# Kernel optimization log

Measured on AMD Instinct MI355X. Metric: run time of the kernel, lower is better.

Reference implementation:

```python
import jax, jax.numpy as jnp
import numpy as np

NN_SIZE = 10  # __init__ default nn_size


def setup_inputs() -> dict:
    key = jax.random.key(0)
    k1, k2 = jax.random.split(key)
    B, N, C = 8, 4096, 3
    xyz1 = jax.random.normal(k1, (B, N, C), dtype=jnp.float32)
    # xyz2 is a small deformation of xyz1 (realistic: deformed shape, same topology)
    xyz2 = xyz1 + 0.05 * jax.random.normal(k2, (B, N, C), dtype=jnp.float32)
    return {"xyz1": xyz1, "xyz2": xyz2}


def _knn_idx(pts, k):
    # brute-force squared-euclidean KNN of pts to itself; pts: (B,N,3) -> idx (B,N,k)
    sq = jnp.sum(pts * pts, axis=-1)                             # (B,N)
    d = sq[:, :, None] - 2.0 * jnp.einsum('bnc,bmc->bnm', pts, pts) + sq[:, None, :]
    _, idx = jax.lax.top_k(-d, k)                                # smallest distances
    return idx


def _point_to_plane(xyz, idx, k):
    # gather neighbors, center, PCA normal from 10x3 SVD, signed point-to-plane dist
    B, N, C = xyz.shape
    grouped = jax.vmap(lambda p, i: p[i])(xyz, idx)              # (B,N,k,3)
    center = jnp.mean(grouped, axis=2, keepdims=True)            # (B,N,1,3)
    local = (grouped - center).reshape(B * N, k, C)              # (B*N,k,3)
    _, _, vh = jnp.linalg.svd(local, full_matrices=False)        # vh: (B*N,3,3)
    # torch V[:, :, -1] == row -1 of Vh: singular vector of smallest singular value
    normals = jax.lax.stop_gradient(vh[:, -1, :].reshape(B, N, C))
    return jnp.sum((xyz - center[:, :, 0, :]) * normals, axis=-1)  # (B,N)


def reference(xyz1, xyz2):
    idx = _knn_idx(xyz1, NN_SIZE)
    ptof1 = _point_to_plane(xyz1, idx, NN_SIZE)
    ptof2 = _point_to_plane(xyz2, idx, NN_SIZE)
    mse = lambda a, b: jnp.mean((a - b) ** 2)
    loss = mse(jnp.abs(ptof1), jnp.abs(ptof2))
    bent = jnp.maximum(ptof2 - ptof1, 0.0)
    loss = loss + 5.0 * mse(bent, jnp.zeros_like(bent))
    return loss
```

## Files before the change

kernel.cpp:

```cpp
#include <hip/hip_runtime.h>
#include <math.h>

#define BB   8
#define NN   4096
#define KK   10
#define TPB  256
#define NPTS (BB * NN)

#define GPP  16
#define PPB  (TPB / GPP)
#define BPBK (NN / PPB)
#define KNBLK (BB * BPBK)
#define TILE 512
#define CAP  32

#define SVDBLK 256
#define SBLK   256

#define LARTG_OLD 0
#define EPSV  5.9604644775390625e-8
#define UNFLV 1.1754943508222875e-38
#define TOLV (10.0 * EPSV)

static __device__ __forceinline__ double lapy2d(double x, double y) {
  double xa = fabs(x), ya = fabs(y);
  double w = fmax(xa, ya), z = fmin(xa, ya);
  if (z == 0.0) return w;
  double q = z / w;
  return w * sqrt(1.0 + q * q);
}

static __device__ __forceinline__ void lartg(double f, double g,
                                             double &c, double &s, double &r) {
#if LARTG_OLD
  if (g == 0.0) { c = 1.0; s = 0.0; r = f; }
  else if (f == 0.0) { c = 0.0; s = 1.0; r = g; }
  else {
    double d = sqrt(f * f + g * g);
    c = f / d; s = g / d; r = d;
    if (fabs(f) > fabs(g) && c < 0.0) { c = -c; s = -s; r = -r; }
  }
#else
  if (g == 0.0) { c = 1.0; s = 0.0; r = f; }
  else if (f == 0.0) { c = 0.0; s = copysign(1.0, g); r = fabs(g); }
  else {
    double d = sqrt(f * f + g * g);
    c = fabs(f) / d;
    r = copysign(d, f);
    s = g / r;
  }
#endif
}

static __device__ void las2(double f, double g, double h, double &ssmin, double &ssmax) {
  double fa = fabs(f), ga = fabs(g), ha = fabs(h);
  double fhmn = fmin(fa, ha), fhmx = fmax(fa, ha);
  if (fhmn == 0.0) {
    ssmin = 0.0;
    if (fhmx == 0.0) ssmax = ga;
    else {
      double mn = fmin(fhmx, ga), mx = fmax(fhmx, ga);
      double rr = mn / mx;
      ssmax = mx * sqrt(1.0 + rr * rr);
    }
  } else {
    if (ga < fhmx) {
      double as_ = 1.0 + fhmn / fhmx;
      double at  = (fhmx - fhmn) / fhmx;
      double au  = (ga / fhmx); au = au * au;
      double c   = 2.0 / (sqrt(as_ * as_ + au) + sqrt(at * at + au));
      ssmin = fhmn * c;
      ssmax = fhmx / c;
    } else {
      double au = fhmx / ga;
      if (au == 0.0) { ssmin = (fhmn * fhmx) / ga; ssmax = ga; }
      else {
        double as_ = 1.0 + fhmn / fhmx;
        double at  = (fhmx - fhmn) / fhmx;
        double t1 = as_ * au, t2 = at * au;
        double c = 1.0 / (sqrt(1.0 + t1 * t1) + sqrt(1.0 + t2 * t2));
        ssmin = (fhmn * c) * au; ssmin = ssmin + ssmin;
        ssmax = ga / (c + c);
      }
    }
  }
}

static __device__ void lasv2(double f, double g, double h,
                             double &ssmin, double &ssmax,
                             double &snr, double &csr, double &snl, double &csl) {
  double ft = f, fa = fabs(f), ht = h, ha = fabs(h);
  int pmax = 1;
  bool swp = (ha > fa);
  if (swp) { pmax = 3; double t = ft; ft = ht; ht = t; t = fa; fa = ha; ha = t; }
  double gt = g, ga = fabs(g);
  double clt = 0, crt = 0, slt = 0, srt = 0;
  if (ga == 0.0) {
    ssmin = ha; ssmax = fa;
    clt = 1.0; crt = 1.0; slt = 0.0; srt = 0.0;
  } else {
    bool gasmal = true;
    if (ga > fa) {
      pmax = 2;
      if ((fa / ga) < EPSV) {
        gasmal = false;
        ssmax = ga;
        if (ha > 1.0) ssmin = fa / (ga / ha);
        else          ssmin = (fa / ga) * ha;
        clt = 1.0; slt = ht / gt; srt = 1.0; crt = ft / gt;
      }
    }
    if (gasmal) {
      double dd = fa - ha, l;
      if (dd == fa) l = 1.0; else l = dd / fa;
      double mv = gt / ft;
      double t = 2.0 - l;
      double mm = mv * mv, tt = t * t;
      double s = sqrt(tt + mm);
      double r = (l == 0.0) ? fabs(mv) : sqrt(l * l + mm);
      double a = 0.5 * (s + r);
      ssmin = ha / a;
      ssmax = fa * a;
      if (mm == 0.0) {
        if (l == 0.0) t = copysign(2.0, ft) * copysign(1.0, gt);
        else          t = gt / copysign(dd, ft) + mv / t;
      } else {
        t = (mv / (s + t) + mv / (r + l)) * (1.0 + a);
      }
      double lq = sqrt(t * t + 4.0);
      crt = 2.0 / lq;
      srt = t / lq;
      clt = (crt + srt * mv) / a;
      slt = (ht / ft) * srt / a;
    }
  }
  if (swp) { csl = srt; snl = crt; csr = slt; snr = clt; }
  else     { csl = clt; snl = slt; csr = crt; snr = srt; }
  double tsign = 1.0;
  if (pmax == 1) tsign = copysign(1.0, csr) * copysign(1.0, csl) * copysign(1.0, f);
  if (pmax == 2) tsign = copysign(1.0, snr) * copysign(1.0, csl) * copysign(1.0, g);
  if (pmax == 3) tsign = copysign(1.0, snr) * copysign(1.0, snl) * copysign(1.0, h);
  ssmax = copysign(ssmax, tsign);
  ssmin = copysign(ssmin, tsign * copysign(1.0, f) * copysign(1.0, h));
}

static __device__ __forceinline__ void rot_rows(double vt[3][3], int lo, double c, double s) {
  if (c != 1.0 || s != 0.0) {
    for (int k = 0; k < 3; ++k) {
      double tp = vt[lo + 1][k];
      vt[lo + 1][k] = c * tp - s * vt[lo][k];
      vt[lo][k]     = s * tp + c * vt[lo][k];
    }
  }
}

static __device__ void bdsqr3(double d[3], double e[2], double vt[3][3]) {
  const double tol = TOLV;
  double sminoa = fabs(d[0]);
  if (sminoa != 0.0) {
    double mu = sminoa;
    mu = fabs(d[1]) * (mu / (mu + fabs(e[0])));
    sminoa = fmin(sminoa, mu);
    if (sminoa != 0.0) {
      mu = fabs(d[2]) * (mu / (mu + fabs(e[1])));
      sminoa = fmin(sminoa, mu);
    }
  }
  sminoa /= sqrt(3.0);
  double thresh = fmax(tol * sminoa, 54.0 * UNFLV);
  int m = 3, oldll = -1, oldm = -1, idir = 0;
  double sminl = 0.0;
  for (int guard = 0; guard < 500 && m > 1; ++guard) {
    double smax = fabs(d[m - 1]);
    int ll = 0;
    bool split = false;
    for (int lll = 1; lll <= m - 1; ++lll) {
      int l = m - lll;
      double abss = fabs(d[l - 1]);
      double abse = fabs(e[l - 1]);
      if (abse <= thresh) { ll = l; split = true; break; }
      smax = fmax(smax, fmax(abss, abse));
    }
    if (split) {
      e[ll - 1] = 0.0;
      if (ll == m - 1) { m = m - 1; continue; }
      ll = ll + 1;
    } else ll = 1;
    if (ll == m - 1) {
      double sigmn, sigmx, sinr, cosr, sinl, cosl;
      lasv2(d[m - 2], e[m - 2], d[m - 1], sigmn, sigmx, sinr, cosr, sinl, cosl);
      d[m - 2] = sigmx; e[m - 2] = 0.0; d[m - 1] = sigmn;
      for (int k = 0; k < 3; ++k) {
        double x = vt[m - 2][k], y = vt[m - 1][k];
        vt[m - 2][k] = cosr * x + sinr * y;
        vt[m - 1][k] = cosr * y - sinr * x;
      }
      m -= 2;
      continue;
    }
    if (ll > oldm || m < oldll)
      idir = (fabs(d[ll - 1]) >= fabs(d[m - 1])) ? 1 : 2;
    bool deflated = false;
    if (idir == 1) {
      if (fabs(e[m - 2]) <= tol * fabs(d[m - 1])) { e[m - 2] = 0.0; continue; }
      double mu = fabs(d[ll - 1]);
      sminl = mu;
      for (int lll = ll; lll <= m - 1; ++lll) {
        if (fabs(e[lll - 1]) <= tol * mu) { e[lll - 1] = 0.0; deflated = true; break; }
        mu = fabs(d[lll]) * (mu / (mu + fabs(e[lll - 1])));
        sminl = fmin(sminl, mu);
      }
    } else {
      if (fabs(e[ll - 1]) <= tol * fabs(d[ll - 1])) { e[ll - 1] = 0.0; continue; }
      double mu = fabs(d[m - 1]);
      sminl = mu;
      for (int lll = m - 1; lll >= ll; --lll) {
        if (fabs(e[lll - 1]) <= tol * mu) { e[lll - 1] = 0.0; deflated = true; break; }
        mu = fabs(d[lll - 1]) * (mu / (mu + fabs(e[lll - 1])));
        sminl = fmin(sminl, mu);
      }
    }
    if (deflated) continue;
    oldll = ll; oldm = m;
    double shift = 0.0, rdum = 0.0;
    if (!(3.0 * tol * (sminl / smax) <= fmax(EPSV, 0.01 * tol))) {
      double sll;
      if (idir == 1) { sll = fabs(d[ll - 1]); las2(d[m - 2], e[m - 2], d[m - 1], shift, rdum); }
      else           { sll = fabs(d[m - 1]); las2(d[ll - 1], e[ll - 1], d[ll], shift, rdum); }
      if (sll > 0.0 && (shift / sll) * (shift / sll) < EPSV) shift = 0.0;
    }
    double csv[2], snv[2];
    if (shift == 0.0) {
      if (idir == 1) {
        double cs = 1.0, oldcs = 1.0, sn = 0.0, oldsn = 0.0, r = 0.0;
        for (int i = ll; i <= m - 1; ++i) {
          lartg(d[i - 1] * cs, e[i - 1], cs, sn, r);
          if (i > ll) e[i - 2] = oldsn * r;
          lartg(oldcs * r, d[i] * sn, oldcs, oldsn, d[i - 1]);
          csv[i - ll] = cs; snv[i - ll] = sn;
        }
        double h = d[m - 1] * cs;
        d[m - 1] = h * oldcs;
        e[m - 2] = h * oldsn;
        for (int j = 0; j <= m - ll - 1; ++j) rot_rows(vt, ll - 1 + j, csv[j], snv[j]);
        if (fabs(e[m - 2]) <= thresh) e[m - 2] = 0.0;
      } else {
        double cs = 1.0, oldcs = 1.0, sn = 0.0, oldsn = 0.0, r = 0.0;
        for (int i = m; i >= ll + 1; --i) {
          lartg(d[i - 1] * cs, e[i - 2], cs, sn, r);
          if (i < m) e[i - 1] = oldsn * r;
          lartg(oldcs * r, d[i - 2] * sn, oldcs, oldsn, d[i - 1]);
          csv[i - ll - 1] = oldcs; snv[i - ll - 1] = -oldsn;
        }
        double h = d[ll - 1] * cs;
        d[ll - 1] = h * oldcs;
        e[ll - 1] = h * oldsn;
        for (int j = m - ll - 1; j >= 0; --j) rot_rows(vt, ll - 1 + j, csv[j], snv[j]);
        if (fabs(e[ll - 1]) <= thresh) e[ll - 1] = 0.0;
      }
    } else {
      if (idir == 1) {
        double f = (fabs(d[ll - 1]) - shift) * (copysign(1.0, d[ll - 1]) + shift / d[ll - 1]);
        double g = e[ll - 1], cosr, sinr, cosl, sinl, r;
        for (int i = ll; i <= m - 1; ++i) {
          lartg(f, g, cosr, sinr, r);
          if (i > ll) e[i - 2] = r;
          f = cosr * d[i - 1] + sinr * e[i - 1];
          e[i - 1] = cosr * e[i - 1] - sinr * d[i - 1];
          g = sinr * d[i];
          d[i] = cosr * d[i];
          lartg(f, g, cosl, sinl, r);
          d[i - 1] = r;
          f = cosl * e[i - 1] + sinl * d[i];
          d[i] = cosl * d[i] - sinl * e[i - 1];
          if (i < m - 1) { g = sinl * e[i]; e[i] = cosl * e[i]; }
          csv[i - ll] = cosr; snv[i - ll] = sinr;
        }
        e[m - 2] = f;
        for (int j = 0; j <= m - ll - 1; ++j) rot_rows(vt, ll - 1 + j, csv[j], snv[j]);
        if (fabs(e[m - 2]) <= thresh) e[m - 2] = 0.0;
      } else {
        double f = (fabs(d[m - 1]) - shift) * (copysign(1.0, d[m - 1]) + shift / d[m - 1]);
        double g = e[m - 2], cosr, sinr, cosl, sinl, r;
        for (int i = m; i >= ll + 1; --i) {
          lartg(f, g, cosr, sinr, r);
          if (i < m) e[i - 1] = r;
          f = cosr * d[i - 1] + sinr * e[i - 2];
          e[i - 2] = cosr * e[i - 2] - sinr * d[i - 1];
          g = sinr * d[i - 2];
          d[i - 2] = cosr * d[i - 2];
          lartg(f, g, cosl, sinl, r);
          d[i - 1] = r;
          f = cosl * e[i - 2] + sinl * d[i - 2];
          d[i - 2] = cosl * d[i - 2] - sinl * e[i - 2];
          if (i > ll + 1) { g = sinl * e[i - 3]; e[i - 3] = cosl * e[i - 3]; }
          csv[i - ll - 1] = cosr; snv[i - ll - 1] = sinr;
        }
        e[ll - 1] = f;
        for (int j = m - ll - 1; j >= 0; --j) rot_rows(vt, ll - 1 + j, csv[j], snv[j]);
        if (fabs(e[ll - 1]) <= thresh) e[ll - 1] = 0.0;
      }
    }
  }
  for (int i = 0; i < 3; ++i)
    if (d[i] < 0.0) { d[i] = -d[i]; for (int k = 0; k < 3; ++k) vt[i][k] = -vt[i][k]; }
}

static __device__ void lapack_normal(double A[KK][3], double &nx, double &ny, double &nz) {
#pragma unroll
  for (int i = 0; i < 3; ++i) {
    double ss = 0.0;
#pragma unroll
    for (int j = i + 1; j < KK; ++j) ss += A[j][i] * A[j][i];
    double xnorm = sqrt(ss);
    if (xnorm != 0.0) {
      double alpha = A[i][i];
      double beta = -copysign(lapy2d(alpha, xnorm), alpha);
      double tau = (beta - alpha) / beta;
      double sc = 1.0 / (alpha - beta);
#pragma unroll
      for (int j = i + 1; j < KK; ++j) A[j][i] *= sc;
      A[i][i] = beta;
#pragma unroll
      for (int c = i + 1; c < 3; ++c) {
        double w = A[i][c];
#pragma unroll
        for (int j = i + 1; j < KK; ++j) w += A[j][i] * A[j][c];
        w *= tau;
        A[i][c] -= w;
#pragma unroll
        for (int j = i + 1; j < KK; ++j) A[j][c] -= w * A[j][i];
      }
    }
  }
  double r11 = A[0][0], r12 = A[0][1], r13 = A[0][2];
  double r22 = A[1][1], r23 = A[1][2], r33 = A[2][2];
  double d[3], e[2];
  double taup1 = 0.0, v3 = 0.0;
  d[0] = r11;
  double a22 = r22, a23 = r23, a32 = 0.0, a33 = r33;
  if (r13 != 0.0) {
    double betap = -copysign(lapy2d(r12, r13), r12);
    taup1 = (betap - r12) / betap;
    v3 = r13 / (r12 - betap);
    e[0] = betap;
    double w2 = (a22 + a23 * v3) * taup1;
    a22 -= w2; a23 -= w2 * v3;
    double w3 = (a33 * v3) * taup1;
    a32 = -w3; a33 -= w3 * v3;
  } else {
    e[0] = r12;
  }
  if (a32 != 0.0) {
    double beta2 = -copysign(lapy2d(a22, a32), a22);
    double tq = (beta2 - a22) / beta2;
    double v2 = a32 / (a22 - beta2);
    d[1] = beta2;
    double w = (a23 + v2 * a33) * tq;
    a23 -= w; a33 -= w * v2;
  } else d[1] = a22;
  e[1] = a23;
  d[2] = a33;
  double vt[3][3] = {{1,0,0},{0,1,0},{0,0,1}};
  bdsqr3(d, e, vt);
  int im = 0;
  if (d[1] < d[im]) im = 1;
  if (d[2] < d[im]) im = 2;
  double w1 = vt[im][0], w2 = vt[im][1], w3 = vt[im][2];
  double sdot = (w2 + w3 * v3) * taup1;
  w2 -= sdot; w3 -= sdot * v3;
  double inv = 1.0 / sqrt(w1 * w1 + w2 * w2 + w3 * w3);
  nx = w1 * inv; ny = w2 * inv; nz = w3 * inv;
}

#define INS2(Kp) { bool lt_ = x < Kp; unsigned long long old_ = Kp; Kp = lt_ ? x : Kp; x = lt_ ? old_ : x; }
#define CSWAP(U,V) { if (V < U) { unsigned long long t_ = U; U = V; V = t_; } }

static __device__ __forceinline__ float dist_dd(float qx, float qy, float qz, float qw,
                                                float xi, float yi, float zi, float sqi) {
  float dot = fmaf(xi, qx, fmaf(yi, qy, __fmul_rn(zi, qz)));
  return fmaf(-2.0f, dot, __fadd_rn(sqi, qw));
}
static __device__ __forceinline__ float sqnorm(float x, float y, float z) {
  return __fadd_rn(__fadd_rn(__fmul_rn(x, x), __fmul_rn(y, y)), __fmul_rn(z, z));
}

__global__ __launch_bounds__(TPB, 1)
void lfl_knn(const float* __restrict__ xyz1, int* __restrict__ idxbuf) {
  __shared__ float4 tile[TILE];
  __shared__ unsigned long long gbuf[PPB][CAP];
  __shared__ unsigned int gcnt[PPB];
  const int t    = threadIdx.x;
  const int b    = blockIdx.x / BPBK;
  const int pb   = blockIdx.x % BPBK;
  const int g    = t >> 4;
  const int sub  = t & 15;
  const int i    = pb * PPB + g;
  const float* base = xyz1 + (size_t)b * NN * 3;

  const float xi  = base[3 * i], yi = base[3 * i + 1], zi = base[3 * i + 2];
  const float sqi = sqnorm(xi, yi, zi);

  float b0 = INFINITY, b1 = INFINITY, b2 = INFINITY;

  for (int t0 = 0; t0 < NN; t0 += TILE) {
    for (int p = t; p < TILE; p += TPB) {
      int j = t0 + p;
      float x = base[3 * j], y = base[3 * j + 1], z = base[3 * j + 2];
      tile[p] = make_float4(x, y, z, sqnorm(x, y, z));
    }
    __syncthreads();
#pragma unroll 4
    for (int c = sub; c < TILE; c += GPP) {
      float4 q = tile[c];
      float x = dist_dd(q.x, q.y, q.z, q.w, xi, yi, zi, sqi);
      float nb0 = fminf(b0, x);
      float nb1 = __builtin_amdgcn_fmed3f(b0, b1, x);
      float nb2 = fminf(b2, fmaxf(b1, x));
      b0 = nb0; b1 = nb1; b2 = nb2;
    }
    __syncthreads();
  }

  float thr;
  {
    float m = b0;
#pragma unroll
    for (int r = 0; r < KK; ++r) {
      m = b0;
      m = fminf(m, __shfl_xor(m, 1));
      m = fminf(m, __shfl_xor(m, 2));
      m = fminf(m, __shfl_xor(m, 4));
      m = fminf(m, __shfl_xor(m, 8));
      if (b0 == m) { b0 = b1; b1 = b2; b2 = INFINITY; }
    }
    thr = m;
  }

  if (sub == 0) gcnt[g] = 0;
  __syncthreads();

  for (int t0 = 0; t0 < NN; t0 += TILE) {
    for (int p = t; p < TILE; p += TPB) {
      int j = t0 + p;
      float x = base[3 * j], y = base[3 * j + 1], z = base[3 * j + 2];
      tile[p] = make_float4(x, y, z, sqnorm(x, y, z));
    }
    __syncthreads();
#pragma unroll 4
    for (int c = sub; c < TILE; c += GPP) {
      float4 q = tile[c];
      float dd = dist_dd(q.x, q.y, q.z, q.w, xi, yi, zi, sqi);
      if (dd <= thr) {
        unsigned u = __float_as_uint(dd);
        u = (u & 0x80000000u) ? ~u : (u | 0x80000000u);
        unsigned long long key = ((unsigned long long)u << 32) | (unsigned)(t0 + c);
        unsigned pos = atomicAdd(&gcnt[g], 1u);
        if (pos < (unsigned)CAP) gbuf[g][pos] = key;
      }
    }
    __syncthreads();
  }

  const unsigned cnt = gcnt[g];
  const int gid = b * NN + i;

  if (cnt <= (unsigned)CAP) {
    unsigned long long e0 = (sub      < (int)cnt) ? gbuf[g][sub]      : ~0ULL;
    unsigned long long e1 = (sub + 16 < (int)cnt) ? gbuf[g][sub + 16] : ~0ULL;
    CSWAP(e0, e1)
#pragma unroll
    for (int r = 0; r < KK; ++r) {
      unsigned long long m = e0, o;
      o = __shfl_xor(m, 1); m = (o < m) ? o : m;
      o = __shfl_xor(m, 2); m = (o < m) ? o : m;
      o = __shfl_xor(m, 4); m = (o < m) ? o : m;
      o = __shfl_xor(m, 8); m = (o < m) ? o : m;
      if (e0 == m) { e0 = e1; e1 = ~0ULL; }
      if (sub == (r & 15)) idxbuf[gid * KK + r] = (int)(unsigned)(m & 0xFFFFFFFFULL);
    }
  } else {
    unsigned long long k0 = ~0ULL, k1 = ~0ULL, k2 = ~0ULL, k3 = ~0ULL, k4 = ~0ULL,
                       k5 = ~0ULL, k6 = ~0ULL, k7 = ~0ULL, k8 = ~0ULL, k9 = ~0ULL;
    for (int c = sub; c < NN; c += GPP) {
      float x = base[3 * c], y = base[3 * c + 1], z = base[3 * c + 2];
      float dd = dist_dd(x, y, z, sqnorm(x, y, z), xi, yi, zi, sqi);
      unsigned u = __float_as_uint(dd);
      u = (u & 0x80000000u) ? ~u : (u | 0x80000000u);
      unsigned long long key = ((unsigned long long)u << 32) | (unsigned)c;
      if (key < k9) {
        unsigned long long x2 = key;
        { unsigned long long &x = x2;
          INS2(k0) INS2(k1) INS2(k2) INS2(k3) INS2(k4)
          INS2(k5) INS2(k6) INS2(k7) INS2(k8) INS2(k9) }
      }
    }
#pragma unroll
    for (int r = 0; r < KK; ++r) {
      unsigned long long m = k0, o;
      o = __shfl_xor(m, 1); m = (o < m) ? o : m;
      o = __shfl_xor(m, 2); m = (o < m) ? o : m;
      o = __shfl_xor(m, 4); m = (o < m) ? o : m;
      o = __shfl_xor(m, 8); m = (o < m) ? o : m;
      if (k0 == m) { k0=k1;k1=k2;k2=k3;k3=k4;k4=k5;k5=k6;k6=k7;k7=k8;k8=k9;k9=~0ULL; }
      if (sub == (r & 15)) idxbuf[gid * KK + r] = (int)(unsigned)(m & 0xFFFFFFFFULL);
    }
  }
}

__global__ __launch_bounds__(TPB, 1)
void lfl_svd(const float* __restrict__ xyz1, const float* __restrict__ xyz2,
             const int* __restrict__ idxbuf, double* __restrict__ partials) {
  __shared__ double pv[TPB];
  __shared__ double red1[128], red2[128];
  const int t = threadIdx.x;
  const int half = t >> 7;
  const int lt = t & 127;
  const int pid = blockIdx.x * 128 + lt;
  const int b = pid / NN, i = pid % NN;
  const float* basep = (half == 0) ? (xyz1 + (size_t)b * NN * 3)
                                   : (xyz2 + (size_t)b * NN * 3);
  double p;
  {
    double A[KK][3];
    double cx = 0, cy = 0, cz = 0;
#pragma unroll
    for (int s = 0; s < KK; ++s) {
      int j = idxbuf[pid * KK + s];
      j = ((unsigned)j < (unsigned)NN) ? j : 0;
      A[s][0] = (double)basep[3 * j];
      A[s][1] = (double)basep[3 * j + 1];
      A[s][2] = (double)basep[3 * j + 2];
      cx += A[s][0]; cy += A[s][1]; cz += A[s][2];
    }
    cx *= 0.1; cy *= 0.1; cz *= 0.1;
#pragma unroll
    for (int s = 0; s < KK; ++s) { A[s][0] -= cx; A[s][1] -= cy; A[s][2] -= cz; }
    double nx, ny, nz;
    lapack_normal(A, nx, ny, nz);
    p = ((double)basep[3 * i] - cx) * nx + ((double)basep[3 * i + 1] - cy) * ny +
        ((double)basep[3 * i + 2] - cz) * nz;
  }
  pv[t] = p;
  __syncthreads();

  if (t < 128) {
    double p1 = pv[t], p2 = pv[t + 128];
    double da = fabs(p1) - fabs(p2);
    double df = p2 - p1;
    double bent = df > 0.0 ? df : 0.0;
    red1[t] = da * da;
    red2[t] = bent * bent;
  }
  __syncthreads();
  for (int s = 64; s > 0; s >>= 1) {
    if (t < s) { red1[t] += red1[t + s]; red2[t] += red2[t + s]; }
    __syncthreads();
  }
  if (t == 0) {
    partials[2 * blockIdx.x]     = red1[0];
    partials[2 * blockIdx.x + 1] = red2[0];
  }
}

__global__ void lfl_final(const double* __restrict__ partials, float* __restrict__ out) {
  if (threadIdx.x == 0 && blockIdx.x == 0) {
    double a = 0.0, bsum = 0.0;
    for (int k = 0; k < SBLK; ++k) {
      a += partials[2 * k];
      bsum += partials[2 * k + 1];
    }
    out[0] = (float)((a + 5.0 * bsum) / (double)NPTS);
  }
}

extern "C" void kernel_launch(void* const* d_in, const int* in_sizes, int n_in,
                              void* d_out, int out_size, void* d_ws, size_t ws_size,
                              hipStream_t stream) {
  const float* xyz1 = (const float*)d_in[0];
  const float* xyz2 = (const float*)d_in[1];
  float* out = (float*)d_out;
  double* partials = (double*)d_ws;
  int* idxbuf = (int*)((char*)d_ws + 4096);

  lfl_knn<<<KNBLK, TPB, 0, stream>>>(xyz1, idxbuf);
  lfl_svd<<<SVDBLK, TPB, 0, stream>>>(xyz1, xyz2, idxbuf, partials);
  lfl_final<<<1, 64, 0, stream>>>(partials, out);
}
```

Measured before the change: 123.0 us.

## Replace per-lane top-3 tracking with four independent running minima in KNN threshold pass

The first KNN pass used to keep a sorted top-3 per lane with a median/min chain. It now keeps four independent running minima, one per interleaved column stream, and sorts them once after the loop. This shortens the dependency chain and cuts ALU work in the hot loop. The threshold it produces is looser, so more candidates pass the filter, which is why the candidate buffer grows from 32 to 48 and the final selection handles three entries per lane. The risk is more atomics in the second pass and more frequent fallbacks to the slow full-scan path.

```diff
diff --git a/kernel.cpp b/kernel.cpp
--- a/kernel.cpp
+++ b/kernel.cpp
@@ -12,7 +12,7 @@
 #define BPBK (NN / PPB)
 #define KNBLK (BB * BPBK)
 #define TILE 512
-#define CAP  32
+#define CAP  48
 
 #define SVDBLK 256
 #define SBLK   256
@@ -374,7 +374,8 @@
 }
 
 #define INS2(Kp) { bool lt_ = x < Kp; unsigned long long old_ = Kp; Kp = lt_ ? x : Kp; x = lt_ ? old_ : x; }
-#define CSWAP(U,V) { if (V < U) { unsigned long long t_ = U; U = V; V = t_; } }
+#define CSWAPU(U,V) { if (V < U) { unsigned long long t_ = U; U = V; V = t_; } }
+#define CSWAPF(U,V) { float mn_ = fminf(U, V); V = fmaxf(U, V); U = mn_; }
 
 static __device__ __forceinline__ float dist_dd(float qx, float qy, float qz, float qw,
                                                 float xi, float yi, float zi, float sqi) {
@@ -401,7 +402,7 @@
   const float xi  = base[3 * i], yi = base[3 * i + 1], zi = base[3 * i + 2];
   const float sqi = sqnorm(xi, yi, zi);
 
-  float b0 = INFINITY, b1 = INFINITY, b2 = INFINITY;
+  float b0 = INFINITY, b1 = INFINITY, b2 = INFINITY, b3 = INFINITY;
 
   for (int t0 = 0; t0 < NN; t0 += TILE) {
     for (int p = t; p < TILE; p += TPB) {
@@ -410,17 +411,19 @@
       tile[p] = make_float4(x, y, z, sqnorm(x, y, z));
     }
     __syncthreads();
-#pragma unroll 4
-    for (int c = sub; c < TILE; c += GPP) {
-      float4 q = tile[c];
-      float x = dist_dd(q.x, q.y, q.z, q.w, xi, yi, zi, sqi);
-      float nb0 = fminf(b0, x);
-      float nb1 = __builtin_amdgcn_fmed3f(b0, b1, x);
-      float nb2 = fminf(b2, fmaxf(b1, x));
-      b0 = nb0; b1 = nb1; b2 = nb2;
+    for (int k = 0; k < TILE / GPP; k += 4) {
+      float4 q0 = tile[sub + (k + 0) * GPP];
+      float4 q1 = tile[sub + (k + 1) * GPP];
+      float4 q2 = tile[sub + (k + 2) * GPP];
+      float4 q3 = tile[sub + (k + 3) * GPP];
+      b0 = fminf(b0, dist_dd(q0.x, q0.y, q0.z, q0.w, xi, yi, zi, sqi));
+      b1 = fminf(b1, dist_dd(q1.x, q1.y, q1.z, q1.w, xi, yi, zi, sqi));
+      b2 = fminf(b2, dist_dd(q2.x, q2.y, q2.z, q2.w, xi, yi, zi, sqi));
+      b3 = fminf(b3, dist_dd(q3.x, q3.y, q3.z, q3.w, xi, yi, zi, sqi));
     }
     __syncthreads();
   }
+  CSWAPF(b0, b1) CSWAPF(b2, b3) CSWAPF(b0, b2) CSWAPF(b1, b3) CSWAPF(b1, b2)
 
   float thr;
   {
@@ -432,7 +435,7 @@
       m = fminf(m, __shfl_xor(m, 2));
       m = fminf(m, __shfl_xor(m, 4));
       m = fminf(m, __shfl_xor(m, 8));
-      if (b0 == m) { b0 = b1; b1 = b2; b2 = INFINITY; }
+      if (b0 == m) { b0 = b1; b1 = b2; b2 = b3; b3 = INFINITY; }
     }
     thr = m;
   }
@@ -468,7 +471,8 @@
   if (cnt <= (unsigned)CAP) {
     unsigned long long e0 = (sub      < (int)cnt) ? gbuf[g][sub]      : ~0ULL;
     unsigned long long e1 = (sub + 16 < (int)cnt) ? gbuf[g][sub + 16] : ~0ULL;
-    CSWAP(e0, e1)
+    unsigned long long e2 = (sub + 32 < (int)cnt) ? gbuf[g][sub + 32] : ~0ULL;
+    CSWAPU(e0, e1) CSWAPU(e1, e2) CSWAPU(e0, e1)
 #pragma unroll
     for (int r = 0; r < KK; ++r) {
       unsigned long long m = e0, o;
@@ -476,7 +480,7 @@
       o = __shfl_xor(m, 2); m = (o < m) ? o : m;
       o = __shfl_xor(m, 4); m = (o < m) ? o : m;
       o = __shfl_xor(m, 8); m = (o < m) ? o : m;
-      if (e0 == m) { e0 = e1; e1 = ~0ULL; }
+      if (e0 == m) { e0 = e1; e1 = e2; e2 = ~0ULL; }
       if (sub == (r & 15)) idxbuf[gid * KK + r] = (int)(unsigned)(m & 0xFFFFFFFFULL);
     }
   } else {
```

Result: faster. 110.6 us (-10.1%).
